# Optimization experiments

Measured on AMD Instinct MI355X. Metric: run time of the kernel, lower is better.

The kernel has to match this reference:

```python
import jax, jax.numpy as jnp
import numpy as np

B, P, F = 512, 512, 1024
EPS = 1e-8


def setup_inputs() -> dict:
    key = jax.random.key(0)
    k1, k2 = jax.random.split(key)
    x = jax.random.normal(k1, (B, F), dtype=jnp.float32)
    # kaiming_normal_(fan_in, relu): std = sqrt(2 / fan_in)
    weight = jax.random.normal(k2, (P, F), dtype=jnp.float32) * np.float32(np.sqrt(2.0 / F))
    bias = jnp.zeros((P,), dtype=jnp.float32)
    alpha = jnp.ones((), dtype=jnp.float32)
    beta = jnp.ones((), dtype=jnp.float32)
    return {"x": x, "weight": weight, "bias": bias, "alpha": alpha, "beta": beta}


def reference(x, weight, bias, alpha, beta):
    # x: (B, F), weight: (P, F)
    x_sig = jax.nn.sigmoid(x)[:, None, :]        # (B, 1, F)
    w_sig = jax.nn.sigmoid(weight)[None, :, :]   # (1, P, F)
    intersection = jnp.minimum(x_sig, w_sig).sum(axis=-1)          # (B, P)
    x_diff = jnp.maximum(x_sig - w_sig, 0.0).sum(axis=-1)          # (B, P)
    w_diff = jnp.maximum(w_sig - x_sig, 0.0).sum(axis=-1)          # (B, P)
    denom = intersection + alpha * x_diff + beta * w_diff + EPS
    return intersection / denom + bias
```

## Files before the change

### kernel.cpp

```cpp
#include <hip/hip_runtime.h>

#define FDIM 1024
#define BDIM 512
#define PDIM 512

__device__ __forceinline__ unsigned sad8(unsigned a, unsigned b, unsigned c) {
  return __builtin_amdgcn_sad_u8(a, b, c);
}

__global__ __launch_bounds__(256) void quant_kernel(
    const float* __restrict__ x, const float* __restrict__ w,
    unsigned* __restrict__ xq, unsigned* __restrict__ wq) {
  const int row = blockIdx.x;
  const int tid = threadIdx.x;
  const bool isx = row < BDIM;
  const float* src = isx ? (x + (size_t)row * FDIM)
                         : (w + (size_t)(row - BDIM) * FDIM);
  float4 v = ((const float4*)src)[tid];
  float s0 = 1.f / (1.f + __expf(-v.x));
  float s1 = 1.f / (1.f + __expf(-v.y));
  float s2 = 1.f / (1.f + __expf(-v.z));
  float s3 = 1.f / (1.f + __expf(-v.w));
  unsigned q0 = (unsigned)(s0 * 255.f + 0.5f);
  unsigned q1 = (unsigned)(s1 * 255.f + 0.5f);
  unsigned q2 = (unsigned)(s2 * 255.f + 0.5f);
  unsigned q3 = (unsigned)(s3 * 255.f + 0.5f);
  unsigned* dq = isx ? (xq + row * (FDIM / 4)) : (wq + (row - BDIM) * (FDIM / 4));
  dq[tid] = q0 | (q1 << 8) | (q2 << 16) | (q3 << 24);
}

__global__ __launch_bounds__(256) void tversky_pair(
    const unsigned* __restrict__ xq, const unsigned* __restrict__ wq,
    const float* __restrict__ bias, const float* __restrict__ alphap,
    const float* __restrict__ betap, float* __restrict__ out) {
  const int tid = threadIdx.x;
  const int lane = tid & 63;
  const int wv = tid >> 6;
  const int r = blockIdx.y * 64 + lane;
  const int c0 = blockIdx.x * 8;

  __shared__ unsigned part[4][8][64];
  __shared__ unsigned sxp[4][64];
  __shared__ unsigned swsum[8];

  if (tid < 8) swsum[tid] = 0;
  __syncthreads();

  const uint4* x4 = (const uint4*)(xq + r * (FDIM / 4) + wv * 64);
  uint4 xv[16];
#pragma unroll
  for (int j = 0; j < 16; ++j) xv[j] = x4[j];

  unsigned sx = 0;
#pragma unroll
  for (int j = 0; j < 16; ++j) {
    sx = sad8(xv[j].x, 0u, sx);
    sx = sad8(xv[j].y, 0u, sx);
    sx = sad8(xv[j].z, 0u, sx);
    sx = sad8(xv[j].w, 0u, sx);
  }
  sxp[wv][lane] = sx;

  {
    const int wrow = tid >> 5;
    const int seg = tid & 31;
    const unsigned* wp = wq + (c0 + wrow) * (FDIM / 4) + seg * 8;
    unsigned s = 0;
#pragma unroll
    for (int j = 0; j < 8; ++j) s = sad8(wp[j], 0u, s);
    atomicAdd(&swsum[wrow], s);
  }

  for (int pp = 0; pp < 8; ++pp) {
    const uint4* w4 = (const uint4*)(wq + (c0 + pp) * (FDIM / 4) + wv * 64);
    unsigned a0 = 0, a1 = 0, a2 = 0, a3 = 0;
#pragma unroll
    for (int j = 0; j < 16; ++j) {
      uint4 ww = w4[j];
      a0 = sad8(xv[j].x, ww.x, a0);
      a1 = sad8(xv[j].y, ww.y, a1);
      a2 = sad8(xv[j].z, ww.z, a2);
      a3 = sad8(xv[j].w, ww.w, a3);
    }
    part[wv][pp][lane] = a0 + a1 + a2 + a3;
  }
  __syncthreads();

  const float alpha = alphap[0];
  const float beta = betap[0];
#pragma unroll
  for (int id = tid; id < 512; id += 256) {
    const int row = id >> 3;
    const int pp = id & 7;
    const unsigned D = part[0][pp][row] + part[1][pp][row] +
                       part[2][pp][row] + part[3][pp][row];
    const unsigned Sxi = sxp[0][row] + sxp[1][row] + sxp[2][row] + sxp[3][row];
    const unsigned Swi = swsum[pp];
    const int b = blockIdx.y * 64 + row;
    const int p = c0 + pp;
    const float fSx = (float)Sxi;
    const float fSw = (float)Swi;
    const float I = 0.5f * (fSx + fSw - (float)D);
    const float denom = I + alpha * (fSx - I) + beta * (fSw - I) + 255.0f * 1e-8f;
    out[b * PDIM + p] = I / denom + bias[p];
  }
}

extern "C" void kernel_launch(void* const* d_in, const int* in_sizes, int n_in,
                              void* d_out, int out_size, void* d_ws, size_t ws_size,
                              hipStream_t stream) {
  const float* x = (const float*)d_in[0];
  const float* w = (const float*)d_in[1];
  const float* bias = (const float*)d_in[2];
  const float* alpha = (const float*)d_in[3];
  const float* beta = (const float*)d_in[4];
  float* out = (float*)d_out;

  unsigned char* ws = (unsigned char*)d_ws;
  unsigned* xq = (unsigned*)ws;
  unsigned* wq = (unsigned*)(ws + 512 * 1024);

  quant_kernel<<<dim3(1024), dim3(256), 0, stream>>>(x, w, xq, wq);
  tversky_pair<<<dim3(PDIM / 8, BDIM / 64), dim3(256), 0, stream>>>(
      xq, wq, bias, alpha, beta, out);
}
```

Before: 76.57 us.

## Store quantized x transposed so pair-kernel x loads coalesce across lanes

New measurement: 72.96 us. 1.05x faster.

```diff
diff --git a/kernel.cpp b/kernel.cpp
--- a/kernel.cpp
+++ b/kernel.cpp
@@ -1,6 +1,7 @@
 #include <hip/hip_runtime.h>
 
 #define FDIM 1024
+#define FD4 256
 #define BDIM 512
 #define PDIM 512
 
@@ -8,15 +9,7 @@
   return __builtin_amdgcn_sad_u8(a, b, c);
 }
 
-__global__ __launch_bounds__(256) void quant_kernel(
-    const float* __restrict__ x, const float* __restrict__ w,
-    unsigned* __restrict__ xq, unsigned* __restrict__ wq) {
-  const int row = blockIdx.x;
-  const int tid = threadIdx.x;
-  const bool isx = row < BDIM;
-  const float* src = isx ? (x + (size_t)row * FDIM)
-                         : (w + (size_t)(row - BDIM) * FDIM);
-  float4 v = ((const float4*)src)[tid];
+__device__ __forceinline__ unsigned quant4(float4 v) {
   float s0 = 1.f / (1.f + __expf(-v.x));
   float s1 = 1.f / (1.f + __expf(-v.y));
   float s2 = 1.f / (1.f + __expf(-v.z));
@@ -25,46 +18,70 @@
   unsigned q1 = (unsigned)(s1 * 255.f + 0.5f);
   unsigned q2 = (unsigned)(s2 * 255.f + 0.5f);
   unsigned q3 = (unsigned)(s3 * 255.f + 0.5f);
-  unsigned* dq = isx ? (xq + row * (FDIM / 4)) : (wq + (row - BDIM) * (FDIM / 4));
-  dq[tid] = q0 | (q1 << 8) | (q2 << 16) | (q3 << 24);
+  return q0 | (q1 << 8) | (q2 << 16) | (q3 << 24);
+}
+
+__global__ __launch_bounds__(256) void quant_kernel(
+    const float* __restrict__ x, const float* __restrict__ w,
+    unsigned* __restrict__ xqT, unsigned* __restrict__ wq) {
+  __shared__ unsigned lt[64 * 65];
+  const int tid = threadIdx.x;
+  if (blockIdx.x < PDIM) {
+    const int row = blockIdx.x;
+    float4 v = ((const float4*)(w + (size_t)row * FDIM))[tid];
+    wq[row * FD4 + tid] = quant4(v);
+  } else {
+    const int t = blockIdx.x - PDIM;
+    const int r0 = (t >> 2) * 64;
+    const int d0 = (t & 3) * 64;
+#pragma unroll
+    for (int j = 0; j < 16; ++j) {
+      const int flat = tid + 256 * j;
+      const int row = flat >> 6;
+      const int c4 = flat & 63;
+      float4 v = ((const float4*)x)[(r0 + row) * FD4 + d0 + c4];
+      lt[row * 65 + c4] = quant4(v);
+    }
+    __syncthreads();
+#pragma unroll
+    for (int j = 0; j < 16; ++j) {
+      const int flat = tid + 256 * j;
+      const int dc = flat >> 6;
+      const int b = flat & 63;
+      xqT[(d0 + dc) * BDIM + r0 + b] = lt[b * 65 + dc];
+    }
+  }
 }
 
 __global__ __launch_bounds__(256) void tversky_pair(
-    const unsigned* __restrict__ xq, const unsigned* __restrict__ wq,
+    const unsigned* __restrict__ xqT, const unsigned* __restrict__ wq,
     const float* __restrict__ bias, const float* __restrict__ alphap,
     const float* __restrict__ betap, float* __restrict__ out) {
   const int tid = threadIdx.x;
   const int lane = tid & 63;
-  const int wv = tid >> 6;
+  const int wv = __builtin_amdgcn_readfirstlane(tid >> 6);
   const int r = blockIdx.y * 64 + lane;
   const int c0 = blockIdx.x * 8;
 
   __shared__ unsigned part[4][8][64];
   __shared__ unsigned sxp[4][64];
   __shared__ unsigned swsum[8];
-
   if (tid < 8) swsum[tid] = 0;
   __syncthreads();
 
-  const uint4* x4 = (const uint4*)(xq + r * (FDIM / 4) + wv * 64);
-  uint4 xv[16];
+  unsigned xv[64];
 #pragma unroll
-  for (int j = 0; j < 16; ++j) xv[j] = x4[j];
+  for (int k = 0; k < 64; ++k) xv[k] = xqT[(wv * 64 + k) * BDIM + r];
 
   unsigned sx = 0;
 #pragma unroll
-  for (int j = 0; j < 16; ++j) {
-    sx = sad8(xv[j].x, 0u, sx);
-    sx = sad8(xv[j].y, 0u, sx);
-    sx = sad8(xv[j].z, 0u, sx);
-    sx = sad8(xv[j].w, 0u, sx);
-  }
+  for (int k = 0; k < 64; ++k) sx = sad8(xv[k], 0u, sx);
   sxp[wv][lane] = sx;
 
   {
     const int wrow = tid >> 5;
     const int seg = tid & 31;
-    const unsigned* wp = wq + (c0 + wrow) * (FDIM / 4) + seg * 8;
+    const unsigned* wp = wq + (c0 + wrow) * FD4 + seg * 8;
     unsigned s = 0;
 #pragma unroll
     for (int j = 0; j < 8; ++j) s = sad8(wp[j], 0u, s);
@@ -72,15 +89,14 @@
   }
 
   for (int pp = 0; pp < 8; ++pp) {
-    const uint4* w4 = (const uint4*)(wq + (c0 + pp) * (FDIM / 4) + wv * 64);
+    const unsigned* wp = wq + (c0 + pp) * FD4 + wv * 64;
     unsigned a0 = 0, a1 = 0, a2 = 0, a3 = 0;
 #pragma unroll
     for (int j = 0; j < 16; ++j) {
-      uint4 ww = w4[j];
-      a0 = sad8(xv[j].x, ww.x, a0);
-      a1 = sad8(xv[j].y, ww.y, a1);
-      a2 = sad8(xv[j].z, ww.z, a2);
-      a3 = sad8(xv[j].w, ww.w, a3);
+      a0 = sad8(xv[4 * j + 0], wp[4 * j + 0], a0);
+      a1 = sad8(xv[4 * j + 1], wp[4 * j + 1], a1);
+      a2 = sad8(xv[4 * j + 2], wp[4 * j + 2], a2);
+      a3 = sad8(xv[4 * j + 3], wp[4 * j + 3], a3);
     }
     part[wv][pp][lane] = a0 + a1 + a2 + a3;
   }
@@ -117,10 +133,10 @@
   float* out = (float*)d_out;
 
   unsigned char* ws = (unsigned char*)d_ws;
-  unsigned* xq = (unsigned*)ws;
+  unsigned* xqT = (unsigned*)ws;
   unsigned* wq = (unsigned*)(ws + 512 * 1024);
 
-  quant_kernel<<<dim3(1024), dim3(256), 0, stream>>>(x, w, xq, wq);
+  quant_kernel<<<dim3(PDIM + 32), dim3(256), 0, stream>>>(x, w, xqT, wq);
   tversky_pair<<<dim3(PDIM / 8, BDIM / 64), dim3(256), 0, stream>>>(
-      xq, wq, bias, alpha, beta, out);
+      xqT, wq, bias, alpha, beta, out);
 }
```
